# Kernel optimization log

Hardware: AMD Instinct MI355X
Metric: run time of the kernel (lower is better)

Reference implementation:

```python
import jax, jax.numpy as jnp
import numpy as np

N, E, IN, H, C = 50000, 500000, 512, 4, 64
NEG_SLOPE = 0.2  # PyG GATConv default LeakyReLU slope


def setup_inputs() -> dict:
    key = jax.random.key(0)
    k = jax.random.split(key, 5)
    x = jax.random.normal(k[0], (N, IN), jnp.float32)
    edge_index = jax.random.randint(k[1], (2, E), 0, N, jnp.int32)
    W = jax.random.normal(k[2], (IN, H * C), jnp.float32) * (1.0 / np.sqrt(IN))
    att_src = jax.random.normal(k[3], (H, C), jnp.float32) * 0.1
    att_dst = jax.random.normal(k[4], (H, C), jnp.float32) * 0.1
    bias = jnp.zeros((H * C,), jnp.float32)
    prelu_a = jnp.full((1,), 0.25, jnp.float32)  # PReLU default init
    return {"x": x, "edge_index": edge_index, "W": W, "att_src": att_src,
            "att_dst": att_dst, "bias": bias, "prelu_a": prelu_a}


def reference(x, edge_index, W, att_src, att_dst, bias, prelu_a):
    n = x.shape[0]
    # add self loops (PyG GATConv default)
    loop = jnp.arange(n, dtype=edge_index.dtype)
    src = jnp.concatenate([edge_index[0], loop])  # message sources j
    dst = jnp.concatenate([edge_index[1], loop])  # aggregation targets i

    h = (x @ W).reshape(n, H, C)                      # [N,H,C]
    a_src = jnp.einsum('nhc,hc->nh', h, att_src)      # [N,H]
    a_dst = jnp.einsum('nhc,hc->nh', h, att_dst)

    e = jax.nn.leaky_relu(a_src[src] + a_dst[dst], NEG_SLOPE)  # [E+N,H]
    m = jax.ops.segment_max(e, dst, num_segments=n)            # per-target max
    e = jnp.exp(e - m[dst])
    denom = jax.ops.segment_sum(e, dst, num_segments=n)
    alpha = e / (denom[dst] + 1e-16)                           # softmax over in-edges

    msgs = alpha[:, :, None] * h[src]                          # [E+N,H,C]
    out = jax.ops.segment_sum(msgs, dst, num_segments=n)       # [N,H,C]
    out = out.reshape(n, H * C) + bias                          # concat heads + bias
    return jnp.where(out >= 0, out, prelu_a * out)              # PReLU
```

## Files before the change

### kernel.cpp

```cpp
#include <hip/hip_runtime.h>
#include <hip/hip_bf16.h>
#include <math.h>

#define IN_DIM 512
#define NHEAD 4
#define CDIM 64
#define HC 256
#define NEG_SLOPE 0.2f
#define GBM 128

typedef __attribute__((ext_vector_type(8))) short bf16x8;
typedef __attribute__((ext_vector_type(4))) float f32x4;

__device__ __forceinline__ unsigned short f2bf_rne(float f) {
    unsigned int u = __float_as_uint(f);
    u = u + 0x7fffu + ((u >> 16) & 1u);
    return (unsigned short)(u >> 16);
}
__device__ __forceinline__ float bf2f(unsigned short h) {
    return __uint_as_float(((unsigned int)h) << 16);
}
__device__ __forceinline__ float readlane_f(float v, int l) {
    return __uint_as_float(__builtin_amdgcn_readlane(__float_as_uint(v), l));
}

__global__ __launch_bounds__(256) void prep_w_kernel(
    const float* __restrict__ W,
    unsigned short* __restrict__ Wp_hi,
    unsigned short* __restrict__ Wp_lo)
{
    int idx = blockIdx.x * 256 + threadIdx.x;
    int slot  = idx & 3;
    int col   = (idx >> 2) & 255;
    int kstep = idx >> 10;
    int kg    = slot ^ ((col >> 1) & 3);
    int kbase = kstep * 32 + kg * 8;
    bf16x8 vh, vl;
#pragma unroll
    for (int e = 0; e < 8; ++e) {
        float f = W[(size_t)(kbase + e) * HC + col];
        unsigned short h = f2bf_rne(f);
        vh[e] = (short)h;
        vl[e] = (short)f2bf_rne(f - bf2f(h));
    }
    size_t off = (size_t)idx * 8;
    *(bf16x8*)(Wp_hi + off) = vh;
    *(bf16x8*)(Wp_lo + off) = vl;
}

__global__ __launch_bounds__(512) void gemm_coef_kernel(
    const float* __restrict__ x,
    const unsigned short* __restrict__ Wp_hi,
    const unsigned short* __restrict__ Wp_lo,
    const float* __restrict__ att_src,
    const float* __restrict__ att_dst,
    float* __restrict__ Hbuf,
    float* __restrict__ a_src,
    float* __restrict__ a_dst,
    int M)
{
    __shared__ char smem[49152];
    char* As_hi = smem;
    char* As_lo = smem + 8192;
    char* Bs_hi = smem + 16384;
    char* Bs_lo = smem + 32768;

    const int tid  = threadIdx.x;
    const int lane = tid & 63;
    const int wv   = tid >> 6;
    const int head = wv & 3;
    const int wrow = (wv >> 2) * 64;
    const int brow = blockIdx.x * GBM;
    const int r16  = lane & 15;
    const int kgrp = lane >> 4;

    f32x4 acc[4][4];
#pragma unroll
    for (int i = 0; i < 4; ++i)
#pragma unroll
        for (int j = 0; j < 4; ++j) acc[i][j] = (f32x4)(0.f);

    const int ar    = tid >> 2;
    const int aslot = tid & 3;

    for (int ks = 0; ks < 16; ++ks) {
        const int k0 = ks * 32;
        {
            const float* src = x + (size_t)(brow + ar) * IN_DIM + k0 + aslot * 8;
            float4 v0 = make_float4(0.f, 0.f, 0.f, 0.f);
            float4 v1 = make_float4(0.f, 0.f, 0.f, 0.f);
            if (brow + ar < M) {
                v0 = *(const float4*)(src);
                v1 = *(const float4*)(src + 4);
            }
            float fv[8] = {v0.x, v0.y, v0.z, v0.w, v1.x, v1.y, v1.z, v1.w};
            bf16x8 vh, vl;
#pragma unroll
            for (int e = 0; e < 8; ++e) {
                unsigned short hh = f2bf_rne(fv[e]);
                vh[e] = (short)hh;
                vl[e] = (short)f2bf_rne(fv[e] - bf2f(hh));
            }
            int addr = ar * 64 + ((aslot ^ ((ar >> 1) & 3)) << 4);
            *(bf16x8*)(As_hi + addr) = vh;
            *(bf16x8*)(As_lo + addr) = vl;
        }
        {
            const char* gh = (const char*)Wp_hi + (size_t)ks * 16384 + wv * 2048;
            const char* gl = (const char*)Wp_lo + (size_t)ks * 16384 + wv * 2048;
#pragma unroll
            for (int i = 0; i < 2; ++i) {
                __builtin_amdgcn_global_load_lds(
                    (const __attribute__((address_space(1))) unsigned int*)(gh + i * 1024 + (lane << 4)),
                    (__attribute__((address_space(3))) unsigned int*)(Bs_hi + wv * 2048 + i * 1024),
                    16, 0, 0);
                __builtin_amdgcn_global_load_lds(
                    (const __attribute__((address_space(1))) unsigned int*)(gl + i * 1024 + (lane << 4)),
                    (__attribute__((address_space(3))) unsigned int*)(Bs_lo + wv * 2048 + i * 1024),
                    16, 0, 0);
            }
        }
        __syncthreads();

        bf16x8 ah[4], al[4], bh[4], bl[4];
#pragma unroll
        for (int fr = 0; fr < 4; ++fr) {
            int row = wrow + fr * 16 + r16;
            int addr = row * 64 + ((kgrp ^ ((row >> 1) & 3)) << 4);
            ah[fr] = *(bf16x8*)(As_hi + addr);
            al[fr] = *(bf16x8*)(As_lo + addr);
        }
#pragma unroll
        for (int fc = 0; fc < 4; ++fc) {
            int col = head * 64 + fc * 16 + r16;
            int addr = col * 64 + ((kgrp ^ ((col >> 1) & 3)) << 4);
            bh[fc] = *(bf16x8*)(Bs_hi + addr);
            bl[fc] = *(bf16x8*)(Bs_lo + addr);
        }
#pragma unroll
        for (int fr = 0; fr < 4; ++fr)
#pragma unroll
            for (int fc = 0; fc < 4; ++fc) {
                acc[fr][fc] = __builtin_amdgcn_mfma_f32_16x16x32_bf16(ah[fr], bh[fc], acc[fr][fc], 0, 0, 0);
                acc[fr][fc] = __builtin_amdgcn_mfma_f32_16x16x32_bf16(ah[fr], bl[fc], acc[fr][fc], 0, 0, 0);
                acc[fr][fc] = __builtin_amdgcn_mfma_f32_16x16x32_bf16(al[fr], bh[fc], acc[fr][fc], 0, 0, 0);
            }
        __syncthreads();
    }

    float asv[4], adv[4];
#pragma unroll
    for (int fc = 0; fc < 4; ++fc) {
        int col = head * 64 + fc * 16 + r16;
        asv[fc] = att_src[col];
        adv[fc] = att_dst[col];
    }
#pragma unroll
    for (int fr = 0; fr < 4; ++fr) {
#pragma unroll
        for (int q = 0; q < 4; ++q) {
            int row = brow + wrow + fr * 16 + kgrp * 4 + q;
            bool ok = row < M;
            float ps = 0.f, pd = 0.f;
#pragma unroll
            for (int fc = 0; fc < 4; ++fc) {
                float v = acc[fr][fc][q];
                if (ok) Hbuf[(size_t)row * HC + head * 64 + fc * 16 + r16] = v;
                ps = fmaf(v, asv[fc], ps);
                pd = fmaf(v, adv[fc], pd);
            }
#pragma unroll
            for (int off = 8; off >= 1; off >>= 1) {
                ps += __shfl_xor(ps, off);
                pd += __shfl_xor(pd, off);
            }
            if (ok && r16 == 0) {
                a_src[row * NHEAD + head] = ps;
                a_dst[row * NHEAD + head] = pd;
            }
        }
    }
}

__global__ void init_deg_kernel(int* deg, int n) {
    int i = blockIdx.x * blockDim.x + threadIdx.x;
    if (i < n) deg[i] = 1;
}
__global__ void count_kernel(const int* __restrict__ dst, int* deg, int e) {
    int i = blockIdx.x * blockDim.x + threadIdx.x;
    if (i < e) atomicAdd(&deg[dst[i]], 1);
}
__global__ __launch_bounds__(256) void scan_block_kernel(
    const int* __restrict__ deg, int* __restrict__ excl,
    int* __restrict__ partials, int n)
{
    __shared__ int s[256];
    int t = threadIdx.x;
    int i = blockIdx.x * 256 + t;
    int v = (i < n) ? deg[i] : 0;
    s[t] = v;
    __syncthreads();
    int x = v;
#pragma unroll
    for (int off = 1; off < 256; off <<= 1) {
        int y = (t >= off) ? s[t - off] : 0;
        __syncthreads();
        x += y;
        s[t] = x;
        __syncthreads();
    }
    if (i < n) excl[i] = x - v;
    if (t == 255) partials[blockIdx.x] = x;
}
__global__ __launch_bounds__(256) void scan_partials_kernel(int* partials, int nb) {
    __shared__ int s[256];
    int t = threadIdx.x;
    int v = (t < nb) ? partials[t] : 0;
    s[t] = v;
    __syncthreads();
    int x = v;
#pragma unroll
    for (int off = 1; off < 256; off <<= 1) {
        int y = (t >= off) ? s[t - off] : 0;
        __syncthreads();
        x += y;
        s[t] = x;
        __syncthreads();
    }
    if (t < nb) partials[t] = x - v;
}
__global__ void add_offsets_kernel(const int* __restrict__ excl,
                                   const int* __restrict__ partials,
                                   int* __restrict__ offs, int n, int total) {
    int i = blockIdx.x * blockDim.x + threadIdx.x;
    if (i < n) offs[i] = excl[i] + partials[i >> 8];
    if (i == 0) offs[n] = total;
}
__global__ void scatter_self_kernel(const int* __restrict__ offs,
                                    int* __restrict__ esrc, int* __restrict__ cursor, int n) {
    int i = blockIdx.x * blockDim.x + threadIdx.x;
    if (i < n) {
        int p = offs[i];
        esrc[p] = i;
        cursor[i] = p + 1;
    }
}
__global__ void scatter_edges_kernel(const int* __restrict__ src, const int* __restrict__ dst,
                                     int* __restrict__ cursor, int* __restrict__ esrc, int e) {
    int i = blockIdx.x * blockDim.x + threadIdx.x;
    if (i < e) {
        int p = atomicAdd(&cursor[dst[i]], 1);
        esrc[p] = src[i];
    }
}

__global__ __launch_bounds__(256) void aggregate_kernel(
    const float* __restrict__ Hbuf,
    const float* __restrict__ a_src,
    const float* __restrict__ a_dst,
    const int* __restrict__ offs,
    const int* __restrict__ esrc,
    const float* __restrict__ bias,
    const float* __restrict__ prelu_a,
    float* __restrict__ out)
{
    int node = blockIdx.x;
    int head = threadIdx.x >> 6;
    int lane = threadIdx.x & 63;

    int beg = offs[node];
    int end = offs[node + 1];
    float adst = a_dst[node * NHEAD + head];
    const float* hb = Hbuf + head * CDIM + lane;

    float d = 0.f;
    float a0 = 0.f, a1 = 0.f, a2 = 0.f, a3 = 0.f;
    for (int c0 = beg; c0 < end; c0 += 64) {
        int j = c0 + lane;
        int s = 0;
        float w = 0.f;
        if (j < end) {
            s = esrc[j];
            float t = a_src[s * NHEAD + head] + adst;
            t = (t >= 0.f) ? t : NEG_SLOPE * t;
            w = __expf(t);
        }
        float cd = w;
#pragma unroll
        for (int off = 32; off >= 1; off >>= 1)
            cd += __shfl_xor(cd, off);
        d += cd;

        int ne = min(64, end - c0);
        int jj = 0;
        for (; jj + 4 <= ne; jj += 4) {
            int   s0 = __builtin_amdgcn_readlane(s, jj + 0);
            int   s1 = __builtin_amdgcn_readlane(s, jj + 1);
            int   s2 = __builtin_amdgcn_readlane(s, jj + 2);
            int   s3 = __builtin_amdgcn_readlane(s, jj + 3);
            float w0 = readlane_f(w, jj + 0);
            float w1 = readlane_f(w, jj + 1);
            float w2 = readlane_f(w, jj + 2);
            float w3 = readlane_f(w, jj + 3);
            float v0 = hb[(size_t)s0 * HC];
            float v1 = hb[(size_t)s1 * HC];
            float v2 = hb[(size_t)s2 * HC];
            float v3 = hb[(size_t)s3 * HC];
            a0 = fmaf(w0, v0, a0);
            a1 = fmaf(w1, v1, a1);
            a2 = fmaf(w2, v2, a2);
            a3 = fmaf(w3, v3, a3);
        }
        for (; jj < ne; ++jj) {
            int   s0 = __builtin_amdgcn_readlane(s, jj);
            float w0 = readlane_f(w, jj);
            a0 = fmaf(w0, hb[(size_t)s0 * HC], a0);
        }
    }
    float o = (a0 + a1 + a2 + a3) / (d + 1e-16f) + bias[head * CDIM + lane];
    float pa = prelu_a[0];
    out[(size_t)node * HC + head * CDIM + lane] = (o >= 0.f) ? o : pa * o;
}

static inline size_t align256(size_t x) { return (x + 255) & ~(size_t)255; }

extern "C" void kernel_launch(void* const* d_in, const int* in_sizes, int n_in,
                              void* d_out, int out_size, void* d_ws, size_t ws_size,
                              hipStream_t stream) {
    const float* x       = (const float*)d_in[0];
    const int*   eidx    = (const int*)d_in[1];
    const float* W       = (const float*)d_in[2];
    const float* att_src = (const float*)d_in[3];
    const float* att_dst = (const float*)d_in[4];
    const float* bias    = (const float*)d_in[5];
    const float* prelu_a = (const float*)d_in[6];
    float* out = (float*)d_out;

    const int N = in_sizes[0] / IN_DIM;
    const int E = in_sizes[1] / 2;
    const int* esrc_in = eidx;
    const int* edst_in = eidx + E;

    char* w = (char*)d_ws;
    unsigned short* Wp_hi = (unsigned short*)w; w += align256((size_t)IN_DIM * HC * 2);
    unsigned short* Wp_lo = (unsigned short*)w; w += align256((size_t)IN_DIM * HC * 2);
    float* Hbuf   = (float*)w; w += align256((size_t)N * HC * 4);
    float* a_srcB = (float*)w; w += align256((size_t)N * NHEAD * 4);
    float* a_dstB = (float*)w; w += align256((size_t)N * NHEAD * 4);
    int*   deg    = (int*)w;   w += align256((size_t)N * 4);
    int*   excl   = (int*)w;   w += align256((size_t)N * 4);
    int*   parts  = (int*)w;   w += align256(256 * 4);
    int*   offs   = (int*)w;   w += align256((size_t)(N + 1) * 4);
    int*   cursor = (int*)w;   w += align256((size_t)N * 4);
    int*   esrc   = (int*)w;   w += align256((size_t)(E + N) * 4);

    prep_w_kernel<<<64, 256, 0, stream>>>(W, Wp_hi, Wp_lo);
    gemm_coef_kernel<<<(N + GBM - 1) / GBM, 512, 0, stream>>>(
        x, Wp_hi, Wp_lo, att_src, att_dst, Hbuf, a_srcB, a_dstB, N);

    {
        int nb = (N + 255) / 256;
        int eb = (E + 255) / 256;
        init_deg_kernel<<<nb, 256, 0, stream>>>(deg, N);
        count_kernel<<<eb, 256, 0, stream>>>(edst_in, deg, E);
        scan_block_kernel<<<nb, 256, 0, stream>>>(deg, excl, parts, N);
        scan_partials_kernel<<<1, 256, 0, stream>>>(parts, nb);
        add_offsets_kernel<<<nb, 256, 0, stream>>>(excl, parts, offs, N, E + N);
        scatter_self_kernel<<<nb, 256, 0, stream>>>(offs, esrc, cursor, N);
        scatter_edges_kernel<<<eb, 256, 0, stream>>>(esrc_in, edst_in, cursor, esrc, E);
    }

    aggregate_kernel<<<N, 256, 0, stream>>>(Hbuf, a_srcB, a_dstB, offs, esrc,
                                            bias, prelu_a, out);
}
```

Before: 354.1 us.

## Double-buffer GEMM B tiles, precompute edge softmax weights during CSR scatter

The GEMM now double-buffers the B tile in shared memory and prefetches the next A slice into registers, so global loads overlap the MFMA work. Edge exponentials are computed once in the scatter kernels, and per-node denominators are accumulated with float atomics. This removes the per-edge exp and wave reductions from the aggregate kernel, which becomes a plain unrolled gather. Small launches are merged: a memset replaces the degree init kernel and the offset and self-loop kernels are fused. The trade-off is extra workspace traffic for the weights and atomic contention on the denominators, and no max-subtraction is applied, so exp could overflow on large logits.

```diff
diff --git a/kernel.cpp b/kernel.cpp
--- a/kernel.cpp
+++ b/kernel.cpp
@@ -20,8 +20,9 @@
 __device__ __forceinline__ float bf2f(unsigned short h) {
     return __uint_as_float(((unsigned int)h) << 16);
 }
-__device__ __forceinline__ float readlane_f(float v, int l) {
-    return __uint_as_float(__builtin_amdgcn_readlane(__float_as_uint(v), l));
+__device__ __forceinline__ float leaky_exp(float t) {
+    t = (t >= 0.f) ? t : NEG_SLOPE * t;
+    return __expf(t);
 }
 
 __global__ __launch_bounds__(256) void prep_w_kernel(
@@ -59,11 +60,9 @@
     float* __restrict__ a_dst,
     int M)
 {
-    __shared__ char smem[49152];
+    __shared__ char smem[81920];
     char* As_hi = smem;
     char* As_lo = smem + 8192;
-    char* Bs_hi = smem + 16384;
-    char* Bs_lo = smem + 32768;
 
     const int tid  = threadIdx.x;
     const int lane = tid & 63;
@@ -74,55 +73,74 @@
     const int r16  = lane & 15;
     const int kgrp = lane >> 4;
 
+    const int  ar      = tid >> 2;
+    const int  aslot   = tid & 3;
+    const bool arow_ok = (brow + ar) < M;
+    const float* aptr  = x + (size_t)(brow + ar) * IN_DIM + aslot * 8;
+    const int  a_addr  = ar * 64 + ((aslot ^ ((ar >> 1) & 3)) << 4);
+
     f32x4 acc[4][4];
 #pragma unroll
     for (int i = 0; i < 4; ++i)
 #pragma unroll
         for (int j = 0; j < 4; ++j) acc[i][j] = (f32x4)(0.f);
 
-    const int ar    = tid >> 2;
-    const int aslot = tid & 3;
+    auto stageB = [&](int ks, int buf) {
+        const char* gh = (const char*)Wp_hi + (size_t)ks * 16384 + wv * 2048 + (lane << 4);
+        const char* gl = (const char*)Wp_lo + (size_t)ks * 16384 + wv * 2048 + (lane << 4);
+        char* lh = smem + 16384 + buf * 32768 + wv * 2048;
+        char* ll = lh + 16384;
+#pragma unroll
+        for (int i = 0; i < 2; ++i) {
+            __builtin_amdgcn_global_load_lds(
+                (const __attribute__((address_space(1))) unsigned int*)(gh + i * 1024),
+                (__attribute__((address_space(3))) unsigned int*)(lh + i * 1024), 16, 0, 0);
+            __builtin_amdgcn_global_load_lds(
+                (const __attribute__((address_space(1))) unsigned int*)(gl + i * 1024),
+                (__attribute__((address_space(3))) unsigned int*)(ll + i * 1024), 16, 0, 0);
+        }
+    };
+    auto loadA = [&](int ks, float4& v0, float4& v1) {
+        v0 = make_float4(0.f, 0.f, 0.f, 0.f);
+        v1 = v0;
+        if (arow_ok) {
+            const float* p = aptr + ks * 32;
+            v0 = *(const float4*)p;
+            v1 = *(const float4*)(p + 4);
+        }
+    };
+    auto writeA = [&](const float4& v0, const float4& v1) {
+        float fv[8] = {v0.x, v0.y, v0.z, v0.w, v1.x, v1.y, v1.z, v1.w};
+        bf16x8 vh, vl;
+#pragma unroll
+        for (int e = 0; e < 8; ++e) {
+            unsigned short hh = f2bf_rne(fv[e]);
+            vh[e] = (short)hh;
+            vl[e] = (short)f2bf_rne(fv[e] - bf2f(hh));
+        }
+        *(bf16x8*)(As_hi + a_addr) = vh;
+        *(bf16x8*)(As_lo + a_addr) = vl;
+    };
+
+    {
+        float4 pv0, pv1;
+        stageB(0, 0);
+        loadA(0, pv0, pv1);
+        writeA(pv0, pv1);
+        __syncthreads();
+    }
 
     for (int ks = 0; ks < 16; ++ks) {
-        const int k0 = ks * 32;
-        {
-            const float* src = x + (size_t)(brow + ar) * IN_DIM + k0 + aslot * 8;
-            float4 v0 = make_float4(0.f, 0.f, 0.f, 0.f);
-            float4 v1 = make_float4(0.f, 0.f, 0.f, 0.f);
-            if (brow + ar < M) {
-                v0 = *(const float4*)(src);
-                v1 = *(const float4*)(src + 4);
-            }
-            float fv[8] = {v0.x, v0.y, v0.z, v0.w, v1.x, v1.y, v1.z, v1.w};
-            bf16x8 vh, vl;
-#pragma unroll
-            for (int e = 0; e < 8; ++e) {
-                unsigned short hh = f2bf_rne(fv[e]);
-                vh[e] = (short)hh;
-                vl[e] = (short)f2bf_rne(fv[e] - bf2f(hh));
-            }
-            int addr = ar * 64 + ((aslot ^ ((ar >> 1) & 3)) << 4);
-            *(bf16x8*)(As_hi + addr) = vh;
-            *(bf16x8*)(As_lo + addr) = vl;
-        }
-        {
-            const char* gh = (const char*)Wp_hi + (size_t)ks * 16384 + wv * 2048;
-            const char* gl = (const char*)Wp_lo + (size_t)ks * 16384 + wv * 2048;
-#pragma unroll
-            for (int i = 0; i < 2; ++i) {
-                __builtin_amdgcn_global_load_lds(
-                    (const __attribute__((address_space(1))) unsigned int*)(gh + i * 1024 + (lane << 4)),
-                    (__attribute__((address_space(3))) unsigned int*)(Bs_hi + wv * 2048 + i * 1024),
-                    16, 0, 0);
-                __builtin_amdgcn_global_load_lds(
-                    (const __attribute__((address_space(1))) unsigned int*)(gl + i * 1024 + (lane << 4)),
-                    (__attribute__((address_space(3))) unsigned int*)(Bs_lo + wv * 2048 + i * 1024),
-                    16, 0, 0);
-            }
-        }
-        __syncthreads();
+        const int cb = ks & 1;
+        float4 nv0, nv1;
+        if (ks < 15) {
+            stageB(ks + 1, cb ^ 1);
+            loadA(ks + 1, nv0, nv1);
+        }
 
         bf16x8 ah[4], al[4], bh[4], bl[4];
+        char* BsH = smem + 16384 + cb * 32768;
+        char* BsL = BsH + 16384;
 #pragma unroll
         for (int fr = 0; fr < 4; ++fr) {
             int row = wrow + fr * 16 + r16;
@@ -134,8 +152,8 @@
         for (int fc = 0; fc < 4; ++fc) {
             int col = head * 64 + fc * 16 + r16;
             int addr = col * 64 + ((kgrp ^ ((col >> 1) & 3)) << 4);
-            bh[fc] = *(bf16x8*)(Bs_hi + addr);
-            bl[fc] = *(bf16x8*)(Bs_lo + addr);
+            bh[fc] = *(bf16x8*)(BsH + addr);
+            bl[fc] = *(bf16x8*)(BsL + addr);
         }
 #pragma unroll
         for (int fr = 0; fr < 4; ++fr)
@@ -145,7 +163,12 @@
                 acc[fr][fc] = __builtin_amdgcn_mfma_f32_16x16x32_bf16(ah[fr], bl[fc], acc[fr][fc], 0, 0, 0);
                 acc[fr][fc] = __builtin_amdgcn_mfma_f32_16x16x32_bf16(al[fr], bh[fc], acc[fr][fc], 0, 0, 0);
             }
-        __syncthreads();
+
+        if (ks < 15) {
+            __syncthreads();
+            writeA(nv0, nv1);
+            __syncthreads();
+        }
     }
 
     float asv[4], adv[4];
@@ -182,10 +205,6 @@
     }
 }
 
-__global__ void init_deg_kernel(int* deg, int n) {
-    int i = blockIdx.x * blockDim.x + threadIdx.x;
-    if (i < n) deg[i] = 1;
-}
 __global__ void count_kernel(const int* __restrict__ dst, int* deg, int e) {
     int i = blockIdx.x * blockDim.x + threadIdx.x;
     if (i < e) atomicAdd(&deg[dst[i]], 1);
@@ -197,7 +216,7 @@
     __shared__ int s[256];
     int t = threadIdx.x;
     int i = blockIdx.x * 256 + t;
-    int v = (i < n) ? deg[i] : 0;
+    int v = (i < n) ? (deg[i] + 1) : 0;
     s[t] = v;
     __syncthreads();
     int x = v;
@@ -229,37 +248,60 @@
     }
     if (t < nb) partials[t] = x - v;
 }
-__global__ void add_offsets_kernel(const int* __restrict__ excl,
-                                   const int* __restrict__ partials,
-                                   int* __restrict__ offs, int n, int total) {
+__global__ void offs_self_kernel(
+    const int* __restrict__ excl, const int* __restrict__ partials,
+    const float* __restrict__ a_src, const float* __restrict__ a_dst,
+    int* __restrict__ offs, int* __restrict__ esrc, int* __restrict__ cursor,
+    float* __restrict__ wexp, float* __restrict__ dsum, int n, int total)
+{
     int i = blockIdx.x * blockDim.x + threadIdx.x;
-    if (i < n) offs[i] = excl[i] + partials[i >> 8];
+    if (i >= n) return;
+    int off = excl[i] + partials[i >> 8];
+    offs[i] = off;
     if (i == 0) offs[n] = total;
-}
-__global__ void scatter_self_kernel(const int* __restrict__ offs,
-                                    int* __restrict__ esrc, int* __restrict__ cursor, int n) {
+    esrc[off] = i;
+    cursor[i] = off + 1;
+    float4 as = *(const float4*)(a_src + (size_t)i * 4);
+    float4 ad = *(const float4*)(a_dst + (size_t)i * 4);
+    float4 w;
+    w.x = leaky_exp(as.x + ad.x);
+    w.y = leaky_exp(as.y + ad.y);
+    w.z = leaky_exp(as.z + ad.z);
+    w.w = leaky_exp(as.w + ad.w);
+    *(float4*)(wexp + (size_t)off * 4) = w;
+    *(float4*)(dsum + (size_t)i * 4) = w;
+}
+__global__ void scatter_edges_kernel(
+    const int* __restrict__ src, const int* __restrict__ dst,
+    const float* __restrict__ a_src, const float* __restrict__ a_dst,
+    int* __restrict__ cursor, int* __restrict__ esrc,
+    float* __restrict__ wexp, float* __restrict__ dsum, int e)
+{
     int i = blockIdx.x * blockDim.x + threadIdx.x;
-    if (i < n) {
-        int p = offs[i];
-        esrc[p] = i;
-        cursor[i] = p + 1;
-    }
-}
-__global__ void scatter_edges_kernel(const int* __restrict__ src, const int* __restrict__ dst,
-                                     int* __restrict__ cursor, int* __restrict__ esrc, int e) {
-    int i = blockIdx.x * blockDim.x + threadIdx.x;
-    if (i < e) {
-        int p = atomicAdd(&cursor[dst[i]], 1);
-        esrc[p] = src[i];
-    }
+    if (i >= e) return;
+    int s  = src[i];
+    int dt = dst[i];
+    int p  = atomicAdd(&cursor[dt], 1);
+    esrc[p] = s;
+    float4 as = *(const float4*)(a_src + (size_t)s * 4);
+    float4 ad = *(const float4*)(a_dst + (size_t)dt * 4);
+    float w0 = leaky_exp(as.x + ad.x);
+    float w1 = leaky_exp(as.y + ad.y);
+    float w2 = leaky_exp(as.z + ad.z);
+    float w3 = leaky_exp(as.w + ad.w);
+    *(float4*)(wexp + (size_t)p * 4) = make_float4(w0, w1, w2, w3);
+    atomicAdd(&dsum[(size_t)dt * 4 + 0], w0);
+    atomicAdd(&dsum[(size_t)dt * 4 + 1], w1);
+    atomicAdd(&dsum[(size_t)dt * 4 + 2], w2);
+    atomicAdd(&dsum[(size_t)dt * 4 + 3], w3);
 }
 
 __global__ __launch_bounds__(256) void aggregate_kernel(
     const float* __restrict__ Hbuf,
-    const float* __restrict__ a_src,
-    const float* __restrict__ a_dst,
     const int* __restrict__ offs,
     const int* __restrict__ esrc,
+    const float* __restrict__ wexp,
+    const float* __restrict__ dsum,
     const float* __restrict__ bias,
     const float* __restrict__ prelu_a,
     float* __restrict__ out)
@@ -270,54 +312,39 @@
 
     int beg = offs[node];
     int end = offs[node + 1];
-    float adst = a_dst[node * NHEAD + head];
+    float d = dsum[(size_t)node * 4 + head];
     const float* hb = Hbuf + head * CDIM + lane;
 
-    float d = 0.f;
     float a0 = 0.f, a1 = 0.f, a2 = 0.f, a3 = 0.f;
-    for (int c0 = beg; c0 < end; c0 += 64) {
-        int j = c0 + lane;
-        int s = 0;
-        float w = 0.f;
-        if (j < end) {
-            s = esrc[j];
-            float t = a_src[s * NHEAD + head] + adst;
-            t = (t >= 0.f) ? t : NEG_SLOPE * t;
-            w = __expf(t);
-        }
-        float cd = w;
-#pragma unroll
-        for (int off = 32; off >= 1; off >>= 1)
-            cd += __shfl_xor(cd, off);
-        d += cd;
-
-        int ne = min(64, end - c0);
-        int jj = 0;
-        for (; jj + 4 <= ne; jj += 4) {
-            int   s0 = __builtin_amdgcn_readlane(s, jj + 0);
-            int   s1 = __builtin_amdgcn_readlane(s, jj + 1);
-            int   s2 = __builtin_amdgcn_readlane(s, jj + 2);
-            int   s3 = __builtin_amdgcn_readlane(s, jj + 3);
-            float w0 = readlane_f(w, jj + 0);
-            float w1 = readlane_f(w, jj + 1);
-            float w2 = readlane_f(w, jj + 2);
-            float w3 = readlane_f(w, jj + 3);
-            float v0 = hb[(size_t)s0 * HC];
-            float v1 = hb[(size_t)s1 * HC];
-            float v2 = hb[(size_t)s2 * HC];
-            float v3 = hb[(size_t)s3 * HC];
-            a0 = fmaf(w0, v0, a0);
-            a1 = fmaf(w1, v1, a1);
-            a2 = fmaf(w2, v2, a2);
-            a3 = fmaf(w3, v3, a3);
-        }
-        for (; jj < ne; ++jj) {
-            int   s0 = __builtin_amdgcn_readlane(s, jj);
-            float w0 = readlane_f(w, jj);
-            a0 = fmaf(w0, hb[(size_t)s0 * HC], a0);
-        }
-    }
-    float o = (a0 + a1 + a2 + a3) / (d + 1e-16f) + bias[head * CDIM + lane];
+    float a4 = 0.f, a5 = 0.f, a6 = 0.f, a7 = 0.f;
+    int j = beg;
+    for (; j + 8 <= end; j += 8) {
+        int s0 = esrc[j + 0], s1 = esrc[j + 1], s2 = esrc[j + 2], s3 = esrc[j + 3];
+        int s4 = esrc[j + 4], s5 = esrc[j + 5], s6 = esrc[j + 6], s7 = esrc[j + 7];
+        float w0 = wexp[(size_t)(j + 0) * 4 + head];
+        float w1 = wexp[(size_t)(j + 1) * 4 + head];
+        float w2 = wexp[(size_t)(j + 2) * 4 + head];
+        float w3 = wexp[(size_t)(j + 3) * 4 + head];
+        float w4 = wexp[(size_t)(j + 4) * 4 + head];
+        float w5 = wexp[(size_t)(j + 5) * 4 + head];
+        float w6 = wexp[(size_t)(j + 6) * 4 + head];
+        float w7 = wexp[(size_t)(j + 7) * 4 + head];
+        a0 = fmaf(w0, hb[(size_t)s0 * HC], a0);
+        a1 = fmaf(w1, hb[(size_t)s1 * HC], a1);
+        a2 = fmaf(w2, hb[(size_t)s2 * HC], a2);
+        a3 = fmaf(w3, hb[(size_t)s3 * HC], a3);
+        a4 = fmaf(w4, hb[(size_t)s4 * HC], a4);
+        a5 = fmaf(w5, hb[(size_t)s5 * HC], a5);
+        a6 = fmaf(w6, hb[(size_t)s6 * HC], a6);
+        a7 = fmaf(w7, hb[(size_t)s7 * HC], a7);
+    }
+    for (; j < end; ++j) {
+        int s0 = esrc[j];
+        float w0 = wexp[(size_t)j * 4 + head];
+        a0 = fmaf(w0, hb[(size_t)s0 * HC], a0);
+    }
+    float acc = ((a0 + a1) + (a2 + a3)) + ((a4 + a5) + (a6 + a7));
+    float o = acc / (d + 1e-16f) + bias[head * CDIM + lane];
     float pa = prelu_a[0];
     out[(size_t)node * HC + head * CDIM + lane] = (o >= 0.f) ? o : pa * o;
 }
@@ -353,7 +380,10 @@
     int*   offs   = (int*)w;   w += align256((size_t)(N + 1) * 4);
     int*   cursor = (int*)w;   w += align256((size_t)N * 4);
     int*   esrc   = (int*)w;   w += align256((size_t)(E + N) * 4);
-
+    float* wexp   = (float*)w; w += align256((size_t)(E + N) * 4 * 4);
+    float* dsum   = (float*)w; w += align256((size_t)N * 4 * 4);
+
+    hipMemsetAsync(deg, 0, (size_t)N * 4, stream);
     prep_w_kernel<<<64, 256, 0, stream>>>(W, Wp_hi, Wp_lo);
     gemm_coef_kernel<<<(N + GBM - 1) / GBM, 512, 0, stream>>>(
         x, Wp_hi, Wp_lo, att_src, att_dst, Hbuf, a_srcB, a_dstB, N);
@@ -361,15 +391,15 @@
     {
         int nb = (N + 255) / 256;
         int eb = (E + 255) / 256;
-        init_deg_kernel<<<nb, 256, 0, stream>>>(deg, N);
         count_kernel<<<eb, 256, 0, stream>>>(edst_in, deg, E);
         scan_block_kernel<<<nb, 256, 0, stream>>>(deg, excl, parts, N);
         scan_partials_kernel<<<1, 256, 0, stream>>>(parts, nb);
-        add_offsets_kernel<<<nb, 256, 0, stream>>>(excl, parts, offs, N, E + N);
-        scatter_self_kernel<<<nb, 256, 0, stream>>>(offs, esrc, cursor, N);
-        scatter_edges_kernel<<<eb, 256, 0, stream>>>(esrc_in, edst_in, cursor, esrc, E);
-    }
-
-    aggregate_kernel<<<N, 256, 0, stream>>>(Hbuf, a_srcB, a_dstB, offs, esrc,
+        offs_self_kernel<<<nb, 256, 0, stream>>>(excl, parts, a_srcB, a_dstB,
+                                                 offs, esrc, cursor, wexp, dsum, N, E + N);
+        scatter_edges_kernel<<<eb, 256, 0, stream>>>(esrc_in, edst_in, a_srcB, a_dstB,
+                                                     cursor, esrc, wexp, dsum, E);
+    }
+
+    aggregate_kernel<<<N, 256, 0, stream>>>(Hbuf, offs, esrc, wexp, dsum,
                                             bias, prelu_a, out);
 }
```

Result: slower. 458.8 us (+29.6%).
